# Optimization experiments

Measured on AMD Instinct MI355X. Metric: run time of the kernel, lower is better.

Reference implementation:

```python
import jax, jax.numpy as jnp
import numpy as np

N, E = 50000, 640000
D_IN, D_OUT, N_BASES = 128, 128, 8


def setup_inputs() -> dict:
    key = jax.random.key(0)
    k1, k2, k3, k4, k5, k6 = jax.random.split(key, 6)
    x = jax.random.normal(k1, (N, D_IN), dtype=jnp.float32)
    edge_index = jax.random.randint(k2, (2, E), 0, N, dtype=jnp.int64)
    # basis-decomposed relation weights (num_relations=1)
    bases = jax.random.normal(k3, (N_BASES, D_IN, D_OUT), dtype=jnp.float32) * 0.05
    comp = jax.random.normal(k4, (1, N_BASES), dtype=jnp.float32)
    root = jax.random.normal(k5, (D_IN, D_OUT), dtype=jnp.float32) * 0.05
    bias = jax.random.normal(k6, (D_OUT,), dtype=jnp.float32) * 0.01
    return {"x": x, "edge_index": edge_index, "bases": bases,
            "comp": comp, "root": root, "bias": bias}


def reference(x, edge_index, bases, comp, root, bias):
    # W[rel=0] = sum_b comp[0,b] * bases[b]  -> [D_IN, D_OUT]
    W = jnp.einsum('b,bio->io', comp[0], bases)
    src = edge_index[0]  # message sources (x_j)
    dst = edge_index[1]  # aggregation targets
    # gather -> scatter-add (aggr='add'), then relation-specific transform
    agg = jax.ops.segment_sum(x[src], dst, num_segments=x.shape[0])  # [N, D_IN]
    out = agg @ W + x @ root + bias  # root/self-loop transform + bias
    return out
```

## Files before the change

kernel.cpp:

```cpp
#include <hip/hip_runtime.h>

#define N_NODES 50000
#define N_EDGES 640000
#define D 128
#define NB 8
#define PAD 32
#define NSTRIP 3125

#define BUCKET_B 256
#define GEMM_B   768

typedef _Float16 half_t;
typedef __attribute__((ext_vector_type(8))) _Float16 half8;
typedef __attribute__((ext_vector_type(4))) float f32x4;

__global__ __launch_bounds__(256)
void init_kernel(const float* __restrict__ bases,
                 const float* __restrict__ comp,
                 const float* __restrict__ root,
                 half_t* __restrict__ Wt,
                 half_t* __restrict__ Rt,
                 half_t* __restrict__ y,
                 int* __restrict__ cnt,
                 int* __restrict__ novf) {
    int i = blockIdx.x * 256 + threadIdx.x;
    if (i == 0) *novf = 0;
    if (i < N_NODES) cnt[i] = 0;
    if (i < D) y[(size_t)N_NODES * D + i] = (half_t)0.f;
    if (i < D * D) {
        int ii = i >> 7, o = i & 127;
        float acc = 0.f;
#pragma unroll
        for (int b = 0; b < NB; ++b)
            acc += comp[b] * bases[((size_t)b * D + ii) * D + o];
        Wt[o * D + ii] = (half_t)acc;
        Rt[o * D + ii] = (half_t)root[i];
    }
}

__global__ __launch_bounds__(256, 4)
void fused_kernel(const float* __restrict__ x,
                  const half_t* __restrict__ Wt,
                  const half_t* __restrict__ Rt,
                  const float* __restrict__ bias,
                  const int* __restrict__ eidx,
                  half_t* __restrict__ y,
                  float* __restrict__ out,
                  int* __restrict__ cnt,
                  int* __restrict__ bucket,
                  int* __restrict__ ovf,
                  int* __restrict__ novf) {
    const int tid = threadIdx.x;

    if (blockIdx.x < BUCKET_B) {
        int t = blockIdx.x * 256 + tid;
        for (int e = t; e < N_EDGES; e += BUCKET_B * 256) {
            int src = eidx[e];
            int dst = eidx[N_EDGES + e];
            int pos = atomicAdd(&cnt[dst], 1);
            if (pos < PAD) {
                bucket[(size_t)dst * PAD + pos] = src;
            } else {
                int k = atomicAdd(novf, 1);
                ovf[2 * k]     = src;
                ovf[2 * k + 1] = dst;
            }
        }
        return;
    }

    const int gb   = blockIdx.x - BUCKET_B;
    const int wave = tid >> 6;
    const int lane = tid & 63;
    const int m    = lane & 15;
    const int quad = lane >> 4;
    const int q    = wave;
    const int s0   = gb;
    const int SSTR = GEMM_B;

    half8 bw[2][4], br[2][4];
    float bb[2];
#pragma unroll
    for (int t = 0; t < 2; ++t) {
        const int nt = 2 * q + t;
        const half_t* wp = Wt + (nt * 16 + m) * D + quad * 8;
        const half_t* rp = Rt + (nt * 16 + m) * D + quad * 8;
#pragma unroll
        for (int kk = 0; kk < 4; ++kk) {
            bw[t][kk] = *(const half8*)(wp + kk * 32);
            br[t][kk] = *(const half8*)(rp + kk * 32);
        }
        bb[t] = bias[nt * 16 + m];
    }

    const float4* x4 = (const float4*)x;
    for (int s = s0; s < NSTRIP; s += SSTR) {
        size_t ab = (size_t)(s * 16 + m) * 32 + quad * 2;
        half8 a[4];
#pragma unroll
        for (int kk = 0; kk < 4; ++kk) {
            float4 v0 = x4[ab + kk * 8];
            float4 v1 = x4[ab + kk * 8 + 1];
            half8 h;
            h[0] = (half_t)v0.x; h[1] = (half_t)v0.y; h[2] = (half_t)v0.z; h[3] = (half_t)v0.w;
            h[4] = (half_t)v1.x; h[5] = (half_t)v1.y; h[6] = (half_t)v1.z; h[7] = (half_t)v1.w;
            a[kk] = h;
        }

        f32x4 accW[2], accR[2];
#pragma unroll
        for (int t = 0; t < 2; ++t) {
            accW[t] = (f32x4){0.f, 0.f, 0.f, 0.f};
            accR[t] = (f32x4){0.f, 0.f, 0.f, 0.f};
        }
#pragma unroll
        for (int t = 0; t < 2; ++t)
#pragma unroll
            for (int kk = 0; kk < 4; ++kk) {
                accW[t] = __builtin_amdgcn_mfma_f32_16x16x32_f16(a[kk], bw[t][kk], accW[t], 0, 0, 0);
                accR[t] = __builtin_amdgcn_mfma_f32_16x16x32_f16(a[kk], br[t][kk], accR[t], 0, 0, 0);
            }

#pragma unroll
        for (int t = 0; t < 2; ++t) {
            int col = (2 * q + t) * 16 + m;
#pragma unroll
            for (int r = 0; r < 4; ++r) {
                int row = s * 16 + quad * 4 + r;
                y[(size_t)row * D + col]   = (half_t)accW[t][r];
                out[(size_t)row * D + col] = accR[t][r] + bb[t];
            }
        }
    }
}

__global__ __launch_bounds__(256)
void gather_kernel(const int* __restrict__ cnt,
                   const int* __restrict__ bucket,
                   const half_t* __restrict__ y,
                   const int* __restrict__ ovf,
                   const int* __restrict__ novf,
                   float* __restrict__ out) {
    const int wave = threadIdx.x >> 6;
    const int lane = threadIdx.x & 63;
    const int g    = lane >> 4;
    const int q    = lane & 15;
    const int node = blockIdx.x * 4 + wave;
    if (node >= N_NODES) return;

    int c_raw = cnt[node];
    int c = c_raw > PAD ? PAD : c_raw;
    const int* bp = bucket + (size_t)node * PAD;

    int base = (c * g) >> 2;
    int ng   = ((c * (g + 1)) >> 2) - base;

    int idx[8];
#pragma unroll
    for (int j = 0; j < 8; ++j)
        idx[j] = (j < ng) ? bp[base + j] : N_NODES;

    half8 v[8];
#pragma unroll
    for (int j = 0; j < 8; ++j)
        v[j] = *(const half8*)(y + (size_t)idx[j] * D + q * 8);

    float acc[8];
#pragma unroll
    for (int t = 0; t < 8; ++t)
        acc[t] = (((float)v[0][t] + (float)v[1][t]) + ((float)v[2][t] + (float)v[3][t]))
               + (((float)v[4][t] + (float)v[5][t]) + ((float)v[6][t] + (float)v[7][t]));

    if (c_raw > PAD) {
        int n = *novf;
        for (int k = g; k < n; k += 4) {
            if (ovf[2 * k + 1] == node) {
                half8 w = *(const half8*)(y + (size_t)ovf[2 * k] * D + q * 8);
#pragma unroll
                for (int t = 0; t < 8; ++t) acc[t] += (float)w[t];
            }
        }
    }

#pragma unroll
    for (int t = 0; t < 8; ++t) {
        acc[t] += __shfl_xor(acc[t], 16);
        acc[t] += __shfl_xor(acc[t], 32);
    }

    if (g == 0) {
        float4* op = (float4*)(out + (size_t)node * D + q * 8);
        float4 o0 = op[0], o1 = op[1];
        o0.x += acc[0]; o0.y += acc[1]; o0.z += acc[2]; o0.w += acc[3];
        o1.x += acc[4]; o1.y += acc[5]; o1.z += acc[6]; o1.w += acc[7];
        op[0] = o0; op[1] = o1;
    }
}

extern "C" void kernel_launch(void* const* d_in, const int* in_sizes, int n_in,
                              void* d_out, int out_size, void* d_ws, size_t ws_size,
                              hipStream_t stream) {
    const float* x     = (const float*)d_in[0];
    const int*   eidx  = (const int*)d_in[1];
    const float* bases = (const float*)d_in[2];
    const float* comp  = (const float*)d_in[3];
    const float* root  = (const float*)d_in[4];
    const float* bias  = (const float*)d_in[5];
    float* out = (float*)d_out;

    char* ws = (char*)d_ws;
    half_t* y      = (half_t*)ws;
    half_t* Wt     = (half_t*)(ws + 12800512);
    half_t* Rt     = (half_t*)(ws + 12833280);
    int*    cnt    = (int*)   (ws + 12866048);
    int*    bucket = (int*)   (ws + 13066048);
    int*    novf   = (int*)   (ws + 19466048);
    int*    ovf    = (int*)   (ws + 19466064);

    init_kernel<<<(N_NODES + 255) / 256, 256, 0, stream>>>(
        bases, comp, root, Wt, Rt, y, cnt, novf);
    fused_kernel<<<BUCKET_B + GEMM_B, 256, 0, stream>>>(
        x, Wt, Rt, bias, eidx, y, out, cnt, bucket, ovf, novf);
    gather_kernel<<<(N_NODES + 3) / 4, 256, 0, stream>>>(
        cnt, bucket, y, ovf, novf, out);
}
```

Baseline: 153.1 us.

## Split edge bucketing by destination half and overlap with gather

Edge bucketing is split in two. The fused GEMM kernel now buckets only edges whose destination is in the first half of the nodes. A new pipe_kernel buckets the second-half edges in extra blocks while the other blocks gather the first-half nodes. A second launch then gathers the second half. The aim is to hide part of the atomic bucketing cost behind gather work, at the price of reading the destination array twice and more launch and scheduling complexity.

New measurement: 153.5 us. About the same (+0.2%).

```diff
diff --git a/kernel.cpp b/kernel.cpp
--- a/kernel.cpp
+++ b/kernel.cpp
@@ -1,6 +1,7 @@
 #include <hip/hip_runtime.h>
 
 #define N_NODES 50000
+#define HALF    25000
 #define N_EDGES 640000
 #define D 128
 #define NB 8
@@ -9,6 +10,7 @@
 
 #define BUCKET_B 256
 #define GEMM_B   768
+#define GBLK_H   6250
 
 typedef _Float16 half_t;
 typedef __attribute__((ext_vector_type(8))) _Float16 half8;
@@ -55,15 +57,17 @@
     if (blockIdx.x < BUCKET_B) {
         int t = blockIdx.x * 256 + tid;
         for (int e = t; e < N_EDGES; e += BUCKET_B * 256) {
-            int src = eidx[e];
             int dst = eidx[N_EDGES + e];
-            int pos = atomicAdd(&cnt[dst], 1);
-            if (pos < PAD) {
-                bucket[(size_t)dst * PAD + pos] = src;
-            } else {
-                int k = atomicAdd(novf, 1);
-                ovf[2 * k]     = src;
-                ovf[2 * k + 1] = dst;
+            if (dst < HALF) {
+                int src = eidx[e];
+                int pos = atomicAdd(&cnt[dst], 1);
+                if (pos < PAD) {
+                    bucket[(size_t)dst * PAD + pos] = src;
+                } else {
+                    int k = atomicAdd(novf, 1);
+                    ovf[2 * k]     = src;
+                    ovf[2 * k + 1] = dst;
+                }
             }
         }
         return;
@@ -75,8 +79,6 @@
     const int m    = lane & 15;
     const int quad = lane >> 4;
     const int q    = wave;
-    const int s0   = gb;
-    const int SSTR = GEMM_B;
 
     half8 bw[2][4], br[2][4];
     float bb[2];
@@ -94,7 +96,7 @@
     }
 
     const float4* x4 = (const float4*)x;
-    for (int s = s0; s < NSTRIP; s += SSTR) {
+    for (int s = gb; s < NSTRIP; s += GEMM_B) {
         size_t ab = (size_t)(s * 16 + m) * 32 + quad * 2;
         half8 a[4];
 #pragma unroll
@@ -134,19 +136,43 @@
     }
 }
 
+template<int BKB, int NODE0>
 __global__ __launch_bounds__(256)
-void gather_kernel(const int* __restrict__ cnt,
-                   const int* __restrict__ bucket,
-                   const half_t* __restrict__ y,
-                   const int* __restrict__ ovf,
-                   const int* __restrict__ novf,
-                   float* __restrict__ out) {
-    const int wave = threadIdx.x >> 6;
-    const int lane = threadIdx.x & 63;
+void pipe_kernel(const int* __restrict__ eidx,
+                 const int* __restrict__ cnt,
+                 const int* __restrict__ bucket,
+                 const half_t* __restrict__ y,
+                 int* __restrict__ ovf,
+                 int* __restrict__ novf,
+                 int* __restrict__ cnt_mut,
+                 float* __restrict__ out) {
+    const int tid = threadIdx.x;
+
+    if (BKB > 0 && blockIdx.x < BKB) {
+        int t = blockIdx.x * 256 + tid;
+        int* bkt = (int*)bucket;
+        for (int e = t; e < N_EDGES; e += BKB * 256) {
+            int dst = eidx[N_EDGES + e];
+            if (dst >= HALF) {
+                int src = eidx[e];
+                int pos = atomicAdd(&cnt_mut[dst], 1);
+                if (pos < PAD) {
+                    bkt[(size_t)dst * PAD + pos] = src;
+                } else {
+                    int k = atomicAdd(novf, 1);
+                    ovf[2 * k]     = src;
+                    ovf[2 * k + 1] = dst;
+                }
+            }
+        }
+        return;
+    }
+
+    const int wave = tid >> 6;
+    const int lane = tid & 63;
     const int g    = lane >> 4;
     const int q    = lane & 15;
-    const int node = blockIdx.x * 4 + wave;
-    if (node >= N_NODES) return;
+    const int node = NODE0 + (blockIdx.x - BKB) * 4 + wave;
 
     int c_raw = cnt[node];
     int c = c_raw > PAD ? PAD : c_raw;
@@ -221,6 +247,8 @@
         bases, comp, root, Wt, Rt, y, cnt, novf);
     fused_kernel<<<BUCKET_B + GEMM_B, 256, 0, stream>>>(
         x, Wt, Rt, bias, eidx, y, out, cnt, bucket, ovf, novf);
-    gather_kernel<<<(N_NODES + 3) / 4, 256, 0, stream>>>(
-        cnt, bucket, y, ovf, novf, out);
-}
+    pipe_kernel<BUCKET_B, 0><<<BUCKET_B + GBLK_H, 256, 0, stream>>>(
+        eidx, cnt, bucket, y, ovf, novf, cnt, out);
+    pipe_kernel<0, HALF><<<GBLK_H, 256, 0, stream>>>(
+        eidx, cnt, bucket, y, ovf, novf, cnt, out);
+}
```
